# Performance work log

Hardware: AMD Instinct MI355X
Metric: run time of the kernel (lower is better)

Reference implementation:

```python
import jax, jax.numpy as jnp
import numpy as np

B, T, C = 4, 2048, 2048
N_HEAD, N_HEAD_KV = 16, 4
HEAD_DIM = C // N_HEAD
ROPE_BASE = 10000.0


def setup_inputs() -> dict:
    key = jax.random.key(0)
    ks = jax.random.split(key, 6)
    x = jax.random.normal(ks[0], (B, T, C), dtype=jnp.float32)
    # freqs_cis: (T, head_dim//2, 2) with [...,0]=cos, [...,1]=sin (true RoPE angles)
    inv_freq = 1.0 / (ROPE_BASE ** (jnp.arange(0, HEAD_DIM, 2, dtype=jnp.float32) / HEAD_DIM))
    angles = jnp.arange(T, dtype=jnp.float32)[:, None] * inv_freq[None, :]  # (T, hd//2)
    freqs_cis = jnp.stack([jnp.cos(angles), jnp.sin(angles)], axis=-1)
    s = 0.02
    Wq = jax.random.normal(ks[1], (C, C), dtype=jnp.float32) * s
    Wk = jax.random.normal(ks[2], (N_HEAD_KV * HEAD_DIM, C), dtype=jnp.float32) * s
    Wv = jax.random.normal(ks[3], (N_HEAD_KV * HEAD_DIM, C), dtype=jnp.float32) * s
    Wo = jax.random.normal(ks[4], (C, C), dtype=jnp.float32) * s
    return {"x": x, "freqs_cis": freqs_cis, "Wq": Wq, "Wk": Wk, "Wv": Wv, "Wo": Wo}


def _rotate_half(u):
    h = u.shape[-1] // 2
    return jnp.concatenate([-u[..., h:], u[..., :h]], axis=-1)


def reference(x, freqs_cis, Wq, Wk, Wv, Wo):
    b, t, c = x.shape
    hd = HEAD_DIM
    q = (x @ Wq.T).reshape(b, t, N_HEAD, hd)
    k = (x @ Wk.T).reshape(b, t, N_HEAD_KV, hd)
    v = (x @ Wv.T).reshape(b, t, N_HEAD_KV, hd)
    # external RoPE (3-dim freqs_cis): cos/sin repeated to full head_dim
    cos = freqs_cis[:t, :, 0]
    sin = freqs_cis[:t, :, 1]
    cos = jnp.concatenate([cos, cos], axis=-1)[None, :, None, :]  # (1,T,1,hd)
    sin = jnp.concatenate([sin, sin], axis=-1)[None, :, None, :]
    q = q * cos + _rotate_half(q) * sin
    k = k * cos + _rotate_half(k) * sin
    # GQA: repeat_interleave kv heads to n_head
    g = N_HEAD // N_HEAD_KV
    k = jnp.repeat(k, g, axis=2)  # (B,T,H,hd)
    v = jnp.repeat(v, g, axis=2)
    scale = 1.0 / np.sqrt(hd)
    scores = jnp.einsum('bthd,bshd->bhts', q, k) * scale  # (B,H,T,S)
    causal = jnp.tril(jnp.ones((t, t), dtype=bool))
    neg = jnp.finfo(scores.dtype).min
    scores = jnp.where(causal[None, None, :, :], scores, neg)
    attn = jax.nn.softmax(scores, axis=-1)
    out = jnp.einsum('bhts,bshd->bthd', attn, v).reshape(b, t, c)
    return out @ Wo.T
```

## Files before the change

### kernel.cpp

```cpp
#include <hip/hip_runtime.h>
#include <hip/hip_bf16.h>
#include <stdint.h>

typedef __bf16 bf16_t;
typedef __bf16 bf16x4 __attribute__((ext_vector_type(4)));
typedef __bf16 bf16x8 __attribute__((ext_vector_type(8)));
typedef float f32x4 __attribute__((ext_vector_type(4)));

__device__ __forceinline__ float fast_exp2(float x) {
#if __has_builtin(__builtin_amdgcn_exp2f)
  return __builtin_amdgcn_exp2f(x);
#else
  return exp2f(x);
#endif
}

__global__ void cvt_all(const float* __restrict__ x,  const float* __restrict__ Wq,
                        const float* __restrict__ Wk, const float* __restrict__ Wv,
                        const float* __restrict__ Wo, bf16_t* __restrict__ xb,
                        bf16_t* __restrict__ wqkv, bf16_t* __restrict__ wob) {
  const int bid = blockIdx.x, tid = threadIdx.x;
  const float* src; bf16_t* dst; int i;
  if (bid < 16384)      { src = x;  dst = xb;             i = bid * 256 + tid; }
  else if (bid < 20480) { src = Wq; dst = wqkv;           i = (bid - 16384) * 256 + tid; }
  else if (bid < 21504) { src = Wk; dst = wqkv + 4194304; i = (bid - 20480) * 256 + tid; }
  else if (bid < 22528) { src = Wv; dst = wqkv + 5242880; i = (bid - 21504) * 256 + tid; }
  else                  { src = Wo; dst = wob;            i = (bid - 22528) * 256 + tid; }
  float4 v = ((const float4*)src)[i];
  bf16x4 o = { (bf16_t)v.x, (bf16_t)v.y, (bf16_t)v.z, (bf16_t)v.w };
  *(bf16x4*)(dst + (size_t)i * 4) = o;
}

__device__ __forceinline__ void async_load16(const bf16_t* g, bf16_t* l) {
#if __has_builtin(__builtin_amdgcn_global_load_lds)
  __builtin_amdgcn_global_load_lds((const __attribute__((address_space(1))) void*)g,
                                   (__attribute__((address_space(3))) void*)l, 16, 0, 0);
#else
  *(bf16x8*)l = *(const bf16x8*)g;
#endif
}

template<bool F32OUT, bool VSPLIT>
__global__ __launch_bounds__(256) void gemm_bt(const bf16_t* __restrict__ A,
                                               const bf16_t* __restrict__ B,
                                               void* __restrict__ C,
                                               bf16_t* __restrict__ Vt,
                                               int M, int N, int K, int ldc,
                                               int vthresh, int vsub) {
  __shared__ bf16_t Alds[128 * 64];
  __shared__ bf16_t Blds[128 * 64];
  const int tid = threadIdx.x;
  const int wave = tid >> 6, lane = tid & 63;
  const int lrow = lane & 15, quad = lane >> 4;
  const int wr = wave >> 1, wc = wave & 1;
  const int bm = blockIdx.y, bn = blockIdx.x;
  const bf16_t* Ab = A + (size_t)bm * 128 * K;
  const bf16_t* Bb = B + (size_t)bn * 128 * K;
  const int r0 = tid >> 3;
  const int c0 = ((tid & 7) ^ (r0 & 7)) << 3;
  f32x4 acc[4][4] = {};

  for (int kk = 0; kk < K; kk += 64) {
#pragma unroll
    for (int p = 0; p < 4; ++p) {
      async_load16(Ab + (size_t)(p * 32 + r0) * K + kk + c0, &Alds[(p * 256 + tid) * 8]);
      async_load16(Bb + (size_t)(p * 32 + r0) * K + kk + c0, &Blds[(p * 256 + tid) * 8]);
    }
    __syncthreads();
#pragma unroll
    for (int ks2 = 0; ks2 < 2; ++ks2) {
      const int rc = ((ks2 * 4 + quad) ^ (lrow & 7)) << 3;
      bf16x8 af[4], bfv[4];
#pragma unroll
      for (int mt = 0; mt < 4; ++mt)
        af[mt] = *(const bf16x8*)&Alds[(wr * 64 + mt * 16 + lrow) * 64 + rc];
#pragma unroll
      for (int nt = 0; nt < 4; ++nt)
        bfv[nt] = *(const bf16x8*)&Blds[(wc * 64 + nt * 16 + lrow) * 64 + rc];
#pragma unroll
      for (int mt = 0; mt < 4; ++mt)
#pragma unroll
        for (int nt = 0; nt < 4; ++nt)
          acc[mt][nt] = __builtin_amdgcn_mfma_f32_16x16x32_bf16(af[mt], bfv[nt], acc[mt][nt], 0, 0, 0);
    }
    __syncthreads();
  }

  if (VSPLIT && bn >= vthresh) {
#pragma unroll
    for (int mt = 0; mt < 4; ++mt)
#pragma unroll
      for (int nt = 0; nt < 4; ++nt) {
        int row = bm * 128 + wr * 64 + mt * 16 + quad * 4;
        int cv  = bn * 128 + wc * 64 + nt * 16 + lrow - vsub;
        int b = row >> 11, tl = row & 2047;
        bf16x4 o;
#pragma unroll
        for (int r = 0; r < 4; ++r) o[r] = (bf16_t)acc[mt][nt][r];
        *(bf16x4*)&Vt[((size_t)(b * 512 + cv)) * 2048 + tl] = o;
      }
    return;
  }
#pragma unroll
  for (int mt = 0; mt < 4; ++mt)
#pragma unroll
    for (int nt = 0; nt < 4; ++nt)
#pragma unroll
      for (int r = 0; r < 4; ++r) {
        int row = bm * 128 + wr * 64 + mt * 16 + quad * 4 + r;
        int col = bn * 128 + wc * 64 + nt * 16 + lrow;
        if (F32OUT) ((float*)C)[(size_t)row * ldc + col] = acc[mt][nt][r];
        else        ((bf16_t*)C)[(size_t)row * ldc + col] = (bf16_t)acc[mt][nt][r];
      }
}

template<bool F32OUT>
__global__ __launch_bounds__(512, 2) void gemm256(const bf16_t* __restrict__ A,
                                                  const bf16_t* __restrict__ B,
                                                  void* __restrict__ C,
                                                  int NBN, int K, int ldc) {
  __shared__ bf16_t As[2][256 * 64];
  __shared__ bf16_t Bs[2][256 * 64];
  const int tid = threadIdx.x;
  const int wave = tid >> 6, lane = tid & 63;
  const int lrow = lane & 15, quad = lane >> 4;
  const int wr = wave >> 2, wc = wave & 3;
  const int nwg = gridDim.x;
  const int wg  = (blockIdx.x & 7) * (nwg >> 3) + (blockIdx.x >> 3);
  const int bm = wg / NBN, bn = wg % NBN;
  const bf16_t* Ag = A + (size_t)bm * 256 * K;
  const bf16_t* Bg = B + (size_t)bn * 256 * K;
  const int srow = tid >> 3;
  const int schunk = (tid & 7) ^ (srow & 7);

  f32x4 acc[2][2][4][2] = {};
  bf16x8 af[4][2], bfr[2][2];
  const int NT = K >> 6;

  auto stageA = [&](int mh, int bsel, int kk) {
#pragma unroll
    for (int i = 0; i < 2; ++i)
      async_load16(Ag + (size_t)(mh * 128 + i * 64 + srow) * K + kk + schunk * 8,
                   &As[bsel][mh * 8192 + i * 4096 + tid * 8]);
  };
  auto stageB = [&](int nh, int bsel, int kk) {
#pragma unroll
    for (int i = 0; i < 2; ++i)
      async_load16(Bg + (size_t)(nh * 128 + i * 64 + srow) * K + kk + schunk * 8,
                   &Bs[bsel][nh * 8192 + i * 4096 + tid * 8]);
  };

#define READ_A(MH)                                                                   \
  _Pragma("unroll")                                                                  \
  for (int mfi = 0; mfi < 4; ++mfi) {                                                \
    const int ra = (MH) * 128 + mfi * 32 + wr * 16 + lrow;                           \
    _Pragma("unroll")                                                                \
    for (int ks = 0; ks < 2; ++ks)                                                   \
      af[mfi][ks] = *(const bf16x8*)&As[buf][ra * 64 +                               \
                        (((ks * 4 + quad) ^ (lrow & 7)) << 3)];                      \
  }
#define READ_B(NH)                                                                   \
  _Pragma("unroll")                                                                  \
  for (int nfi = 0; nfi < 2; ++nfi) {                                                \
    const int rb = (NH) * 128 + nfi * 64 + wc * 16 + lrow;                           \
    _Pragma("unroll")                                                                \
    for (int ks = 0; ks < 2; ++ks)                                                   \
      bfr[nfi][ks] = *(const bf16x8*)&Bs[buf][rb * 64 +                              \
                         (((ks * 4 + quad) ^ (lrow & 7)) << 3)];                     \
  }
#define MFMA_Q(MH, NH)                                                               \
  __builtin_amdgcn_s_setprio(1);                                                     \
  _Pragma("unroll")                                                                  \
  for (int ks = 0; ks < 2; ++ks)                                                     \
    _Pragma("unroll")                                                                \
    for (int mfi = 0; mfi < 4; ++mfi)                                                \
      _Pragma("unroll")                                                              \
      for (int nfi = 0; nfi < 2; ++nfi)                                              \
        acc[MH][NH][mfi][nfi] = __builtin_amdgcn_mfma_f32_16x16x32_bf16(             \
            af[mfi][ks], bfr[nfi][ks], acc[MH][NH][mfi][nfi], 0, 0, 0);              \
  __builtin_amdgcn_s_setprio(0);

  stageA(0, 0, 0);
  stageB(0, 0, 0);
  stageB(1, 0, 0);
  stageA(1, 0, 0);
  asm volatile("s_waitcnt vmcnt(4)" ::: "memory");
  __builtin_amdgcn_s_barrier();

  for (int t = 0; t < NT; ++t) {
    const int buf = t & 1, obuf = buf ^ 1;
    const int kn = (t + 1) << 6;
    const bool pf = (t + 1 < NT);
    READ_A(0)
    READ_B(0)
    if (pf) stageA(0, obuf, kn);
    __builtin_amdgcn_s_barrier();
    asm volatile("s_waitcnt lgkmcnt(0)" ::: "memory");
    MFMA_Q(0, 0)
    if (pf) asm volatile("s_waitcnt vmcnt(4)" ::: "memory");
    else    asm volatile("s_waitcnt vmcnt(2)" ::: "memory");
    __builtin_amdgcn_s_barrier();
    READ_B(1)
    if (pf) stageB(0, obuf, kn);
    __builtin_amdgcn_s_barrier();
    asm volatile("s_waitcnt lgkmcnt(0)" ::: "memory");
    MFMA_Q(0, 1)
    if (pf) asm volatile("s_waitcnt vmcnt(4)" ::: "memory");
    else    asm volatile("s_waitcnt vmcnt(0)" ::: "memory");
    __builtin_amdgcn_s_barrier();
    READ_A(1)
    if (pf) stageB(1, obuf, kn);
    __builtin_amdgcn_s_barrier();
    asm volatile("s_waitcnt lgkmcnt(0)" ::: "memory");
    MFMA_Q(1, 1)
    __builtin_amdgcn_s_barrier();
    READ_B(0)
    if (pf) stageA(1, obuf, kn);
    __builtin_amdgcn_s_barrier();
    asm volatile("s_waitcnt lgkmcnt(0)" ::: "memory");
    MFMA_Q(1, 0)
    if (pf) asm volatile("s_waitcnt vmcnt(4)" ::: "memory");
    __builtin_amdgcn_s_barrier();
  }
#undef READ_A
#undef READ_B
#undef MFMA_Q

#pragma unroll
  for (int mh = 0; mh < 2; ++mh)
#pragma unroll
    for (int nh = 0; nh < 2; ++nh)
#pragma unroll
      for (int mfi = 0; mfi < 4; ++mfi)
#pragma unroll
        for (int nfi = 0; nfi < 2; ++nfi)
#pragma unroll
          for (int r = 0; r < 4; ++r) {
            int row = bm * 256 + mh * 128 + mfi * 32 + wr * 16 + quad * 4 + r;
            int col = bn * 256 + nh * 128 + nfi * 64 + wc * 16 + lrow;
            if (F32OUT) ((float*)C)[(size_t)row * ldc + col] = acc[mh][nh][mfi][nfi][r];
            else        ((bf16_t*)C)[(size_t)row * ldc + col] = (bf16_t)acc[mh][nh][mfi][nfi][r];
          }
}

__global__ void rope_kernel(bf16_t* __restrict__ X, const float* __restrict__ F,
                            int hshift, int stride) {
  int i = blockIdx.x * blockDim.x + threadIdx.x;
  int d = i & 63;
  int h = (i >> 6) & ((1 << hshift) - 1);
  int row = i >> (6 + hshift);
  int t = row & 2047;
  float c = F[t * 128 + d * 2];
  float s = F[t * 128 + d * 2 + 1];
  size_t base = (size_t)row * stride + h * 128 + d;
  float q0 = (float)X[base];
  float q1 = (float)X[base + 64];
  X[base]      = (bf16_t)(q0 * c - q1 * s);
  X[base + 64] = (bf16_t)(q1 * c + q0 * s);
}

__global__ __launch_bounds__(256, 2) void attn_kernel(const bf16_t* __restrict__ QKV,
                                                      const float* __restrict__ F,
                                                      const bf16_t* __restrict__ Vt,
                                                      bf16_t* __restrict__ O) {
  __shared__ bf16_t Ks[2][64 * 128];
  __shared__ bf16_t Vs[2][128 * 64];
  __shared__ bf16_t Ps[4 * 32 * 64];
  const int tid = threadIdx.x;
  const int wave = tid >> 6, lane = tid & 63;
  const int lrow = lane & 15, quad = lane >> 4;
  const int bh = blockIdx.y, b = bh >> 4, h = bh & 15, kvh = h >> 2;
  const size_t qoff  = ((size_t)b * 2048) * 2560 + (size_t)h * 128;
  const size_t koff  = ((size_t)b * 2048) * 2560 + 2048 + (size_t)kvh * 128;
  const size_t vtoff = ((size_t)(b * 4 + kvh) * 128) * 2048;
  const float qsc = 0.08838834764831845f * 1.44269504088896340736f;
  bf16_t* Pw = Ps + wave * (32 * 64);
  const float2* F2 = (const float2*)F;

  const int krow_l = tid >> 4;
  const int kdc    = (tid & 15) ^ (krow_l & 7);
  const int vrow_l = tid >> 3;
  const int vkc    = (tid & 7) ^ (vrow_l & 7);

  auto stage = [&](int kt, int bsel) {
    const bf16_t* Kg = QKV + koff + (size_t)(kt * 64) * 2560;
    const bf16_t* Vg = Vt + vtoff + kt * 64;
    bf16_t* Kd = &Ks[bsel][0];
    bf16_t* Vd = &Vs[bsel][0];
#pragma unroll
    for (int c4 = 0; c4 < 4; ++c4) {
      int ci = c4 * 256 + tid;
      async_load16(Kg + (size_t)(c4 * 16 + krow_l) * 2560 + kdc * 8, Kd + ci * 8);
      async_load16(Vg + (size_t)(c4 * 32 + vrow_l) * 2048 + vkc * 8, Vd + ci * 8);
    }
  };

  for (int phase = 0; phase < 2; ++phase) {
    const int qt = phase ? (15 - blockIdx.x) : blockIdx.x;
    const int qbase = qt * 128 + wave * 32;

    bf16x8 qf[2][4];
#pragma unroll
    for (int nt2 = 0; nt2 < 2; ++nt2) {
      const int t = qbase + nt2 * 16 + lrow;
      const bf16_t* qp = QKV + qoff + (size_t)t * 2560 + quad * 8;
      bf16x8 raw[4];
#pragma unroll
      for (int ks = 0; ks < 4; ++ks) raw[ks] = *(const bf16x8*)(qp + ks * 32);
#pragma unroll
      for (int ks2 = 0; ks2 < 2; ++ks2) {
        bf16x8 lo, hi;
#pragma unroll
        for (int j = 0; j < 8; ++j) {
          int d = ks2 * 32 + quad * 8 + j;
          float2 cs = F2[t * 64 + d];
          float q0 = (float)raw[ks2][j], q1 = (float)raw[ks2 + 2][j];
          lo[j] = (bf16_t)((q0 * cs.x - q1 * cs.y) * qsc);
          hi[j] = (bf16_t)((q1 * cs.x + q0 * cs.y) * qsc);
        }
        qf[nt2][ks2]     = lo;
        qf[nt2][ks2 + 2] = hi;
      }
    }

    f32x4 Oacc[2][8] = {};
    float m_r[2] = {-1.0e30f, -1.0e30f};
    float l_r[2] = {0.f, 0.f};
    const int kt_end = 2 * qt + 2;

    stage(0, 0);

    for (int kt = 0; kt < kt_end; ++kt) {
      __syncthreads();
      if (kt + 1 < kt_end) stage(kt + 1, (kt + 1) & 1);
      const bf16_t* Kb_ = &Ks[kt & 1][0];
      const bf16_t* Vb_ = &Vs[kt & 1][0];

      if (kt * 64 <= qbase + 31) {
        f32x4 S[2][4] = {};
#pragma unroll
        for (int ks = 0; ks < 4; ++ks) {
          bf16x8 kf[4];
#pragma unroll
          for (int mt = 0; mt < 4; ++mt) {
            int dc = (ks * 4 + quad) ^ (lrow & 7);
            kf[mt] = *(const bf16x8*)&Kb_[(mt * 16 + lrow) * 128 + dc * 8];
          }
#pragma unroll
          for (int nt2 = 0; nt2 < 2; ++nt2)
#pragma unroll
            for (int mt = 0; mt < 4; ++mt)
              S[nt2][mt] = __builtin_amdgcn_mfma_f32_16x16x32_bf16(kf[mt], qf[nt2][ks], S[nt2][mt], 0, 0, 0);
        }
        if (kt * 64 + 63 > qbase) {
#pragma unroll
          for (int nt2 = 0; nt2 < 2; ++nt2) {
            int q = qbase + nt2 * 16 + lrow;
#pragma unroll
            for (int mt = 0; mt < 4; ++mt) {
              int key0 = kt * 64 + mt * 16 + quad * 4;
#pragma unroll
              for (int r = 0; r < 4; ++r)
                if (key0 + r > q) S[nt2][mt][r] = -1.0e30f;
            }
          }
        }
        float alpha[2];
#pragma unroll
        for (int nt2 = 0; nt2 < 2; ++nt2) {
          float mx = -1.0e30f;
#pragma unroll
          for (int mt = 0; mt < 4; ++mt)
#pragma unroll
            for (int r = 0; r < 4; ++r) mx = fmaxf(mx, S[nt2][mt][r]);
          mx = fmaxf(mx, __shfl_xor(mx, 16, 64));
          mx = fmaxf(mx, __shfl_xor(mx, 32, 64));
          float mold = m_r[nt2];
          float mnew = (mx - mold <= 8.0f) ? mold : mx;
          alpha[nt2] = fast_exp2(mold - mnew);
          m_r[nt2] = mnew;
          float rs = 0.f;
          const int prow = nt2 * 16 + lrow;
          const int pbase = prow * 64 + ((quad & 1) << 2);
#pragma unroll
          for (int mt = 0; mt < 4; ++mt) {
            bf16x4 pk;
#pragma unroll
            for (int r = 0; r < 4; ++r) {
              float p = fast_exp2(S[nt2][mt][r] - mnew);
              rs += p;
              pk[r] = (bf16_t)p;
            }
            int c8 = ((mt * 2 + (quad >> 1)) ^ (prow & 7)) << 3;
            *(bf16x4*)&Pw[pbase + c8] = pk;
          }
          rs += __shfl_xor(rs, 16, 64);
          rs += __shfl_xor(rs, 32, 64);
          l_r[nt2] = l_r[nt2] * alpha[nt2] + rs;
        }
        bool nz = (alpha[0] != 1.f) || (alpha[1] != 1.f);
        if (__ballot(nz) != 0ull) {
#pragma unroll
          for (int mt2 = 0; mt2 < 2; ++mt2)
#pragma unroll
            for (int r = 0; r < 4; ++r) {
              float av = __shfl(alpha[mt2], quad * 4 + r, 16);
#pragma unroll
              for (int dt = 0; dt < 8; ++dt) Oacc[mt2][dt][r] *= av;
            }
        }
#pragma unroll
        for (int ks2 = 0; ks2 < 2; ++ks2) {
          bf16x8 ap[2];
#pragma unroll
          for (int mt2 = 0; mt2 < 2; ++mt2) {
            int prow = mt2 * 16 + lrow;
            ap[mt2] = *(const bf16x8*)&Pw[prow * 64 + (((ks2 * 4 + quad) ^ (prow & 7)) << 3)];
          }
          int dc = (ks2 * 4 + quad) ^ (lrow & 7);
#pragma unroll
          for (int dt = 0; dt < 8; ++dt) {
            bf16x8 bv = *(const bf16x8*)&Vb_[(dt * 16 + lrow) * 64 + dc * 8];
#pragma unroll
            for (int mt2 = 0; mt2 < 2; ++mt2)
              Oacc[mt2][dt] = __builtin_amdgcn_mfma_f32_16x16x32_bf16(ap[mt2], bv, Oacc[mt2][dt], 0, 0, 0);
          }
        }
      }
    }

#pragma unroll
    for (int mt2 = 0; mt2 < 2; ++mt2)
#pragma unroll
      for (int r = 0; r < 4; ++r) {
        float lv = __shfl(l_r[mt2], quad * 4 + r, 16);
        float inv = 1.0f / lv;
        int row = qbase + mt2 * 16 + quad * 4 + r;
#pragma unroll
        for (int dt = 0; dt < 8; ++dt)
          O[(size_t)b * 2048 * 2048 + (size_t)row * 2048 + h * 128 + dt * 16 + lrow] =
              (bf16_t)(Oacc[mt2][dt][r] * inv);
      }
  }
}

extern "C" void kernel_launch(void* const* d_in, const int* in_sizes, int n_in,
                              void* d_out, int out_size, void* d_ws, size_t ws_size,
                              hipStream_t stream) {
  const float* x  = (const float*)d_in[0];
  const float* fc = (const float*)d_in[1];
  const float* Wq = (const float*)d_in[2];
  const float* Wk = (const float*)d_in[3];
  const float* Wv = (const float*)d_in[4];
  const float* Wo = (const float*)d_in[5];
  float* out = (float*)d_out;

  char* ws = (char*)d_ws;
  size_t off = 0;
  auto alloc = [&](size_t bytes) { char* p = ws + off; off += bytes; return p; };
  bf16_t* xb    = (bf16_t*)alloc((size_t)8192 * 2048 * 2);
  bf16_t* Wqkvb = (bf16_t*)alloc((size_t)3072 * 2048 * 2);
  bf16_t* Wob   = (bf16_t*)alloc((size_t)2048 * 2048 * 2);
  bf16_t* QKVb  = (bf16_t*)alloc((size_t)8192 * 2560 * 2);
  bf16_t* Ab    = (bf16_t*)alloc((size_t)8192 * 2048 * 2);
  bf16_t* Vtb   = (bf16_t*)alloc((size_t)2048 * 2048 * 2);
  (void)ws_size; (void)in_sizes; (void)n_in; (void)out_size;

  cvt_all<<<26624, 256, 0, stream>>>(x, Wq, Wk, Wv, Wo, xb, Wqkvb, Wob);

  gemm256<false><<<256, 512, 0, stream>>>(xb, Wqkvb, QKVb, 8, 2048, 2560);

  gemm_bt<false, true><<<dim3(8, 64), 256, 0, stream>>>(
      xb, Wqkvb + (size_t)2048 * 2048, QKVb + 2048, Vtb, 8192, 1024, 2048, 2560, 4, 512);

  rope_kernel<<<8192, 256, 0, stream>>>(QKVb + 2048, fc, 2, 2560);

  attn_kernel<<<dim3(8, 64), 256, 0, stream>>>(QKVb, fc, Vtb, Ab);

  gemm256<true><<<256, 512, 0, stream>>>(Ab, Wob, out, 8, 2048, 2048);
}
```

Measured before the change: 434.6 us.

## Interleave softmax and PV MFMA per row group; merge QKV projection into one GEMM

The attention inner loop now processes each 16-row query group end to end: max, exp, rescale, then the P·V MFMAs. The other group's softmax can then overlap with this group's matrix work, and fewer alpha values stay live. The QKV projection drops the separate 256-tile GEMM for Q and runs a single gemm_bt launch over all 3072 output columns, including the V transpose path. This removes a launch, but the Q projection now runs on the smaller-tile kernel, which may be less efficient than gemm256. It also issues a ballot per group rather than one.

```diff
diff --git a/kernel.cpp b/kernel.cpp
--- a/kernel.cpp
+++ b/kernel.cpp
@@ -365,29 +365,29 @@
             }
           }
         }
-        float alpha[2];
-#pragma unroll
-        for (int nt2 = 0; nt2 < 2; ++nt2) {
+
+#pragma unroll
+        for (int g = 0; g < 2; ++g) {
           float mx = -1.0e30f;
 #pragma unroll
           for (int mt = 0; mt < 4; ++mt)
 #pragma unroll
-            for (int r = 0; r < 4; ++r) mx = fmaxf(mx, S[nt2][mt][r]);
+            for (int r = 0; r < 4; ++r) mx = fmaxf(mx, S[g][mt][r]);
           mx = fmaxf(mx, __shfl_xor(mx, 16, 64));
           mx = fmaxf(mx, __shfl_xor(mx, 32, 64));
-          float mold = m_r[nt2];
+          float mold = m_r[g];
           float mnew = (mx - mold <= 8.0f) ? mold : mx;
-          alpha[nt2] = fast_exp2(mold - mnew);
-          m_r[nt2] = mnew;
+          float alpha = fast_exp2(mold - mnew);
+          m_r[g] = mnew;
           float rs = 0.f;
-          const int prow = nt2 * 16 + lrow;
+          const int prow = g * 16 + lrow;
           const int pbase = prow * 64 + ((quad & 1) << 2);
 #pragma unroll
           for (int mt = 0; mt < 4; ++mt) {
             bf16x4 pk;
 #pragma unroll
             for (int r = 0; r < 4; ++r) {
-              float p = fast_exp2(S[nt2][mt][r] - mnew);
+              float p = fast_exp2(S[g][mt][r] - mnew);
               rs += p;
               pk[r] = (bf16_t)p;
             }
@@ -396,34 +396,28 @@
           }
           rs += __shfl_xor(rs, 16, 64);
           rs += __shfl_xor(rs, 32, 64);
-          l_r[nt2] = l_r[nt2] * alpha[nt2] + rs;
-        }
-        bool nz = (alpha[0] != 1.f) || (alpha[1] != 1.f);
-        if (__ballot(nz) != 0ull) {
-#pragma unroll
-          for (int mt2 = 0; mt2 < 2; ++mt2)
+          l_r[g] = l_r[g] * alpha + rs;
+
+          if (__ballot(alpha != 1.f) != 0ull) {
 #pragma unroll
             for (int r = 0; r < 4; ++r) {
-              float av = __shfl(alpha[mt2], quad * 4 + r, 16);
-#pragma unroll
-              for (int dt = 0; dt < 8; ++dt) Oacc[mt2][dt][r] *= av;
+              float av = __shfl(alpha, quad * 4 + r, 16);
+#pragma unroll
+              for (int dt = 0; dt < 8; ++dt) Oacc[g][dt][r] *= av;
             }
-        }
-#pragma unroll
-        for (int ks2 = 0; ks2 < 2; ++ks2) {
-          bf16x8 ap[2];
-#pragma unroll
-          for (int mt2 = 0; mt2 < 2; ++mt2) {
-            int prow = mt2 * 16 + lrow;
-            ap[mt2] = *(const bf16x8*)&Pw[prow * 64 + (((ks2 * 4 + quad) ^ (prow & 7)) << 3)];
-          }
-          int dc = (ks2 * 4 + quad) ^ (lrow & 7);
-#pragma unroll
-          for (int dt = 0; dt < 8; ++dt) {
-            bf16x8 bv = *(const bf16x8*)&Vb_[(dt * 16 + lrow) * 64 + dc * 8];
-#pragma unroll
-            for (int mt2 = 0; mt2 < 2; ++mt2)
-              Oacc[mt2][dt] = __builtin_amdgcn_mfma_f32_16x16x32_bf16(ap[mt2], bv, Oacc[mt2][dt], 0, 0, 0);
+          }
+
+#pragma unroll
+          for (int ks2 = 0; ks2 < 2; ++ks2) {
+            const int prow_g = g * 16 + lrow;
+            bf16x8 ap = *(const bf16x8*)&Pw[prow_g * 64 +
+                            (((ks2 * 4 + quad) ^ (prow_g & 7)) << 3)];
+            int dc = (ks2 * 4 + quad) ^ (lrow & 7);
+#pragma unroll
+            for (int dt = 0; dt < 8; ++dt) {
+              bf16x8 bv = *(const bf16x8*)&Vb_[(dt * 16 + lrow) * 64 + dc * 8];
+              Oacc[g][dt] = __builtin_amdgcn_mfma_f32_16x16x32_bf16(ap, bv, Oacc[g][dt], 0, 0, 0);
+            }
           }
         }
       }
@@ -468,10 +462,8 @@
 
   cvt_all<<<26624, 256, 0, stream>>>(x, Wq, Wk, Wv, Wo, xb, Wqkvb, Wob);
 
-  gemm256<false><<<256, 512, 0, stream>>>(xb, Wqkvb, QKVb, 8, 2048, 2560);
-
-  gemm_bt<false, true><<<dim3(8, 64), 256, 0, stream>>>(
-      xb, Wqkvb + (size_t)2048 * 2048, QKVb + 2048, Vtb, 8192, 1024, 2048, 2560, 4, 512);
+  gemm_bt<false, true><<<dim3(24, 64), 256, 0, stream>>>(
+      xb, Wqkvb, QKVb, Vtb, 8192, 3072, 2048, 2560, 20, 2560);
 
   rope_kernel<<<8192, 256, 0, stream>>>(QKVb + 2048, fc, 2, 2560);
 
```

After: 437.4 us. About the same (+0.7%).

## Merge Q/K/V projections into one launch and fuse K RoPE into epilogue

Applied to the files above, without the earlier changes.

Replaces the separate Q GEMM (256x256 tiles), the K/V GEMM and the standalone RoPE kernel with a single 128x128-tile gemm_bt launch covering all Q, K and V columns. For K tiles, the B-fragment column mapping is permuted so each lane holds both halves d and d+64 of a head, which lets the epilogue apply RoPE before writing. This removes two kernel launches and the extra read-modify-write pass over K, but Q now runs on the smaller 128 tile GEMM instead of the larger-tile gemm256 kernel, which may lower GEMM efficiency.

```diff
diff --git a/kernel.cpp b/kernel.cpp
--- a/kernel.cpp
+++ b/kernel.cpp
@@ -45,7 +45,8 @@
                                                const bf16_t* __restrict__ B,
                                                void* __restrict__ C,
                                                bf16_t* __restrict__ Vt,
-                                               int M, int N, int K, int ldc,
+                                               const float* __restrict__ F,
+                                               int K, int ldc,
                                                int vthresh, int vsub) {
   __shared__ bf16_t Alds[128 * 64];
   __shared__ bf16_t Blds[128 * 64];
@@ -54,6 +55,9 @@
   const int lrow = lane & 15, quad = lane >> 4;
   const int wr = wave >> 1, wc = wave & 1;
   const int bm = blockIdx.y, bn = blockIdx.x;
+  const bool isK = VSPLIT && (bn >= 16) && (bn < vthresh);
+  const int nns = isK ? 32 : 16;
+  const int ncs = isK ? 16 : 64;
   const bf16_t* Ab = A + (size_t)bm * 128 * K;
   const bf16_t* Bb = B + (size_t)bn * 128 * K;
   const int r0 = tid >> 3;
@@ -76,7 +80,7 @@
         af[mt] = *(const bf16x8*)&Alds[(wr * 64 + mt * 16 + lrow) * 64 + rc];
 #pragma unroll
       for (int nt = 0; nt < 4; ++nt)
-        bfv[nt] = *(const bf16x8*)&Blds[(wc * 64 + nt * 16 + lrow) * 64 + rc];
+        bfv[nt] = *(const bf16x8*)&Blds[(wc * ncs + nt * nns + lrow) * 64 + rc];
 #pragma unroll
       for (int mt = 0; mt < 4; ++mt)
 #pragma unroll
@@ -98,6 +102,27 @@
 #pragma unroll
         for (int r = 0; r < 4; ++r) o[r] = (bf16_t)acc[mt][nt][r];
         *(bf16x4*)&Vt[((size_t)(b * 512 + cv)) * 2048 + tl] = o;
+      }
+    return;
+  }
+  if (isK) {
+    const float2* F2 = (const float2*)F;
+    bf16_t* Cb = (bf16_t*)C;
+#pragma unroll
+    for (int mt = 0; mt < 4; ++mt)
+#pragma unroll
+      for (int nt = 0; nt < 2; ++nt) {
+        const int d_lo = wc * 16 + nt * 32 + lrow;
+        const int col  = bn * 128 + d_lo;
+#pragma unroll
+        for (int r = 0; r < 4; ++r) {
+          int row = bm * 128 + wr * 64 + mt * 16 + quad * 4 + r;
+          int t = row & 2047;
+          float2 cs = F2[t * 64 + d_lo];
+          float q0 = acc[mt][nt][r], q1 = acc[mt][nt + 2][r];
+          Cb[(size_t)row * ldc + col]      = (bf16_t)(q0 * cs.x - q1 * cs.y);
+          Cb[(size_t)row * ldc + col + 64] = (bf16_t)(q1 * cs.x + q0 * cs.y);
+        }
       }
     return;
   }
@@ -243,22 +268,6 @@
           }
 }
 
-__global__ void rope_kernel(bf16_t* __restrict__ X, const float* __restrict__ F,
-                            int hshift, int stride) {
-  int i = blockIdx.x * blockDim.x + threadIdx.x;
-  int d = i & 63;
-  int h = (i >> 6) & ((1 << hshift) - 1);
-  int row = i >> (6 + hshift);
-  int t = row & 2047;
-  float c = F[t * 128 + d * 2];
-  float s = F[t * 128 + d * 2 + 1];
-  size_t base = (size_t)row * stride + h * 128 + d;
-  float q0 = (float)X[base];
-  float q1 = (float)X[base + 64];
-  X[base]      = (bf16_t)(q0 * c - q1 * s);
-  X[base + 64] = (bf16_t)(q1 * c + q0 * s);
-}
-
 __global__ __launch_bounds__(256, 2) void attn_kernel(const bf16_t* __restrict__ QKV,
                                                       const float* __restrict__ F,
                                                       const bf16_t* __restrict__ Vt,
@@ -468,12 +477,9 @@
 
   cvt_all<<<26624, 256, 0, stream>>>(x, Wq, Wk, Wv, Wo, xb, Wqkvb, Wob);
 
-  gemm256<false><<<256, 512, 0, stream>>>(xb, Wqkvb, QKVb, 8, 2048, 2560);
-
-  gemm_bt<false, true><<<dim3(8, 64), 256, 0, stream>>>(
-      xb, Wqkvb + (size_t)2048 * 2048, QKVb + 2048, Vtb, 8192, 1024, 2048, 2560, 4, 512);
-
-  rope_kernel<<<8192, 256, 0, stream>>>(QKVb + 2048, fc, 2, 2560);
+  gemm_bt<false, true><<<dim3(24, 64), 256, 0, stream>>>(
+      xb, Wqkvb, QKVb, Vtb, fc, 2048, 2560, 20, 2560);
+
 
   attn_kernel<<<dim3(8, 64), 256, 0, stream>>>(QKVb, fc, Vtb, Ab);
 
```

New measurement: 442.5 us. Within noise of the previous version (+1.8%).
